# Performance work log

Hardware: AMD Instinct MI355X
Metric: run time of the kernel (lower is better)

Reference implementation:

```python
import jax, jax.numpy as jnp
import numpy as np

D = 1024
H = 16
FFN = 4096
B = 4
S = 1024
EPS = 1e-12
NEG = -1e9


def _layernorm(x, gamma, beta):
    mean = x.mean(-1, keepdims=True)
    var = ((x - mean) ** 2).mean(-1, keepdims=True)  # biased var, matches unbiased=False
    return gamma * (x - mean) * jax.lax.rsqrt(var + EPS) + beta


def setup_inputs() -> dict:
    key = jax.random.key(0)
    ks = jax.random.split(key, 16)
    s_in = 1.0 / np.sqrt(D)
    s_ff = 1.0 / np.sqrt(FFN)
    return {
        "x": jax.random.normal(ks[0], (B, S, D), dtype=jnp.float32),
        "mask": jax.random.randint(ks[1], (B, H, S), 0, 2) > 0,  # bernoulli(0.5) key mask
        "Wqkv": jax.random.uniform(ks[2], (3 * D, D), minval=-s_in, maxval=s_in),
        "bqkv": jax.random.uniform(ks[3], (3 * D,), minval=-s_in, maxval=s_in),
        "Wo": jax.random.uniform(ks[4], (D, D), minval=-s_in, maxval=s_in),
        "bo": jax.random.uniform(ks[5], (D,), minval=-s_in, maxval=s_in),
        "W1": jax.random.uniform(ks[6], (FFN, D), minval=-s_in, maxval=s_in),
        "b1": jax.random.uniform(ks[7], (FFN,), minval=-s_in, maxval=s_in),
        "W2": jax.random.uniform(ks[8], (D, FFN), minval=-s_ff, maxval=s_ff),
        "b2": jax.random.uniform(ks[9], (D,), minval=-s_ff, maxval=s_ff),
        "g1": jnp.ones((D,), jnp.float32),
        "be1": jnp.zeros((D,), jnp.float32),
        "g2": jnp.ones((D,), jnp.float32),
        "be2": jnp.zeros((D,), jnp.float32),
    }


def reference(x, mask, Wqkv, bqkv, Wo, bo, W1, b1, W2, b2, g1, be1, g2, be2):
    b, s, _ = x.shape
    hd = D // H
    scale = hd ** -0.5

    # --- ProbSparseSelfAttention (dropout in eval mode) ---
    qkv = x @ Wqkv.T + bqkv                                   # [b, s, 3D]
    q, k, v = jnp.split(qkv, 3, axis=-1)
    q = q.reshape(b, s, H, hd).transpose(0, 2, 1, 3)          # [b, h, s, d]
    k = k.reshape(b, s, H, hd).transpose(0, 2, 1, 3)
    v = v.reshape(b, s, H, hd).transpose(0, 2, 1, 3)
    scores = jnp.einsum('bhid,bhjd->bhij', q * scale, k)      # [b, h, s, s]
    scores = jnp.where(mask[:, :, None, :], scores, NEG)      # mask keys (broadcast over i)
    attn = jax.nn.softmax(scores, axis=-1)
    ctx = jnp.einsum('bhij,bhjd->bhid', attn, v)
    ctx = ctx.transpose(0, 2, 1, 3).reshape(b, s, D)
    attn_out = ctx @ Wo.T + bo

    # residual + LayerNorm 1
    h = _layernorm(attn_out + x, g1, be1)

    # --- FFN ---
    ff = jax.nn.relu(h @ W1.T + b1) @ W2.T + b2

    # residual + LayerNorm 2
    return _layernorm(ff + h, g2, be2)
```

## Files before the change

### kernel.cpp

```cpp
#include <hip/hip_runtime.h>

#define DDIM 1024
#define FFN_DIM 4096
#define SS 1024
#define MTOK 4096

typedef __bf16 bf16x8 __attribute__((ext_vector_type(8)));
typedef float f32x4 __attribute__((ext_vector_type(4)));
typedef unsigned short ushort4v __attribute__((ext_vector_type(4)));
typedef unsigned short ushort8v __attribute__((ext_vector_type(8)));

__device__ __forceinline__ unsigned short f2bf(float f) {
    __bf16 h = (__bf16)f;
    return __builtin_bit_cast(unsigned short, h);
}
__device__ __forceinline__ float bf2f(unsigned short u) {
    union { unsigned u; float f; } x;
    x.u = (unsigned)u << 16;
    return x.f;
}

__device__ __forceinline__ int swz(int off) {
    return off ^ ((((off >> 7) & 7) ^ ((off >> 10) & 1)) << 4);
}
__device__ __forceinline__ int gswz(int b) {
    return b ^ (((b >> 7) & 7) << 4);
}

__device__ __forceinline__ void gload_lds16(const void* g, void* l) {
    __builtin_amdgcn_global_load_lds(
        (__attribute__((address_space(1))) unsigned int*)(unsigned long long)(g),
        (__attribute__((address_space(3))) unsigned int*)(l), 16, 0, 0);
}

__global__ __launch_bounds__(256) void cvt_all(const float* __restrict__ x,
                                               const float* __restrict__ wqkv,
                                               const float* __restrict__ wo,
                                               const float* __restrict__ w1,
                                               const float* __restrict__ w2,
                                               unsigned short* __restrict__ xbf,
                                               unsigned short* __restrict__ wqkvb,
                                               unsigned short* __restrict__ wob,
                                               unsigned short* __restrict__ w1b,
                                               unsigned short* __restrict__ w2b) {
    int i = blockIdx.x * 256 + threadIdx.x;
    const float* src;
    unsigned short* dst;
    int off;
    if (i < 1048576)      { src = x;    dst = xbf;   off = i; }
    else if (i < 1835008) { src = wqkv; dst = wqkvb; off = i - 1048576; }
    else if (i < 2097152) { src = wo;   dst = wob;   off = i - 1835008; }
    else if (i < 3145728) { src = w1;   dst = w1b;   off = i - 2097152; }
    else                  { src = w2;   dst = w2b;   off = i - 3145728; }
    float4 v = ((const float4*)src)[off];
    ushort4v u = {f2bf(v.x), f2bf(v.y), f2bf(v.z), f2bf(v.w)};
    ((ushort4v*)dst)[off] = u;
}

template <int EPI, int SPLITK>
__global__ __launch_bounds__(512, 2) void gemm256(const unsigned short* __restrict__ A,
                                                  const unsigned short* __restrict__ B,
                                                  const float* __restrict__ bias,
                                                  unsigned short* __restrict__ O0,
                                                  unsigned short* __restrict__ O1,
                                                  unsigned short* __restrict__ O2,
                                                  unsigned short* __restrict__ O3,
                                                  int M, int N, int K) {
    __shared__ char smem[131072];
    const int tid = threadIdx.x;
    const int wid = tid >> 6, lane = tid & 63;
    const int wm = wid >> 2, wn = wid & 3;
    const int lr = lane & 15, lkb = (lane >> 4) * 16;
    const int m0 = blockIdx.y * 256, n0 = blockIdx.x * 256;
    const int z = blockIdx.z;
    const int Kc = K / SPLITK, kb = z * Kc;
    const int NT = Kc / 64;

    f32x4 acc[8][4];
#pragma unroll
    for (int i = 0; i < 8; i++)
#pragma unroll
        for (int j = 0; j < 4; j++) acc[i][j] = (f32x4){0.f, 0.f, 0.f, 0.f};

    auto stage_tile = [&](int c, int t) {
        const int k0 = kb + t * 64;
#pragma unroll
        for (int hs = 0; hs < 4; ++hs) {
            const int op = hs >> 1, h = hs & 1;
            const unsigned short* G = op ? B : A;
            const int r0 = (op ? n0 : m0) + h * 128;
            char* base = smem + c * 65536 + op * 32768 + h * 16384;
#pragma unroll
            for (int q = 0; q < 2; q++) {
                int d = q * 8192 + wid * 1024 + lane * 16;
                int s = gswz(d);
                gload_lds16(G + (size_t)(r0 + (s >> 7)) * K + k0 + ((s & 127) >> 1),
                            base + q * 8192 + wid * 1024);
            }
        }
    };

    stage_tile(0, 0);
    asm volatile("s_waitcnt vmcnt(0)" ::: "memory");
    __syncthreads();

    for (int t = 0; t < NT; ++t) {
        const int c = t & 1;
        const char* Ab = smem + c * 65536;
        const char* Bb = Ab + 32768;
        const bool pre = (t + 1 < NT);
        bf16x8 bfr[4][2];
#pragma unroll
        for (int p = 0; p < 4; ++p) {
            bf16x8 afr[2][2];
#pragma unroll
            for (int mi = 0; mi < 2; mi++)
#pragma unroll
                for (int ks = 0; ks < 2; ks++) {
                    int b = (wm * 128 + (p * 2 + mi) * 16 + lr) * 128 + ks * 64 + lkb;
                    afr[mi][ks] = *(const bf16x8*)(Ab + gswz(b));
                }
            if (p == 0) {
#pragma unroll
                for (int nb = 0; nb < 4; nb++)
#pragma unroll
                    for (int ks = 0; ks < 2; ks++) {
                        int b = (wn * 64 + nb * 16 + lr) * 128 + ks * 64 + lkb;
                        bfr[nb][ks] = *(const bf16x8*)(Bb + gswz(b));
                    }
                if (pre) stage_tile(c ^ 1, t + 1);
            }
            __builtin_amdgcn_s_barrier();
            asm volatile("s_waitcnt lgkmcnt(0)" ::: "memory");
            __builtin_amdgcn_sched_barrier(0);
            __builtin_amdgcn_s_setprio(1);
#pragma unroll
            for (int mi = 0; mi < 2; mi++)
#pragma unroll
                for (int nb = 0; nb < 4; nb++)
#pragma unroll
                    for (int ks = 0; ks < 2; ks++)
                        acc[p * 2 + mi][nb] = __builtin_amdgcn_mfma_f32_16x16x32_bf16(
                            afr[mi][ks], bfr[nb][ks], acc[p * 2 + mi][nb], 0, 0, 0);
            __builtin_amdgcn_s_setprio(0);
            if (p == 3 && pre) asm volatile("s_waitcnt vmcnt(0)" ::: "memory");
            __builtin_amdgcn_s_barrier();
        }
    }

    unsigned short* Op = (SPLITK == 1) ? O0 : (z == 0 ? O0 : z == 1 ? O1 : z == 2 ? O2 : O3);
    float bv[4];
#pragma unroll
    for (int nb = 0; nb < 4; nb++) bv[nb] = (z == 0) ? bias[n0 + wn * 64 + nb * 16 + lr] : 0.f;
    const int rr = (lane >> 4) * 4;
#pragma unroll
    for (int mb = 0; mb < 8; mb++)
#pragma unroll
        for (int nb = 0; nb < 4; nb++) {
            int col = n0 + wn * 64 + nb * 16 + lr;
#pragma unroll
            for (int r = 0; r < 4; r++) {
                int row = m0 + wm * 128 + mb * 16 + rr + r;
                float v = acc[mb][nb][r] + bv[nb];
                if (EPI == 2) v = fmaxf(v, 0.f);
                Op[(size_t)row * N + col] = f2bf(v);
            }
        }
}

__global__ __launch_bounds__(256) void gemm_bt(const unsigned short* __restrict__ A,
                                               const unsigned short* __restrict__ B,
                                               const float* __restrict__ bias,
                                               unsigned short* __restrict__ Cout,
                                               int M, int N, int K) {
    __shared__ unsigned short Asm[2][128 * 32];
    __shared__ unsigned short Bsm[2][128 * 32];
    const int tid = threadIdx.x;
    const int wid = tid >> 6, lane = tid & 63;
    const int m0 = blockIdx.y * 128, n0 = blockIdx.x * 128;
    const int lr = lane & 15, lk = (lane >> 4) * 8;
    const int wr = (wid >> 1) * 64, wc = (wid & 1) * 64;
    const int nkt = K / 32;

    f32x4 acc[4][4];
#pragma unroll
    for (int i = 0; i < 4; i++)
#pragma unroll
        for (int j = 0; j < 4; j++) acc[i][j] = (f32x4){0.f, 0.f, 0.f, 0.f};

    const unsigned short* Ag = A + (size_t)m0 * K;
    const unsigned short* Bg = B + (size_t)n0 * K;

    auto stage = [&](int buf, int k0) {
#pragma unroll
        for (int p = 0; p < 2; ++p) {
            int idx = p * 4096 + wid * 1024 + lane * 16;
            int row = idx >> 6, ce = (idx & 63) >> 1;
            gload_lds16(Ag + (size_t)row * K + k0 + ce, (char*)Asm[buf] + p * 4096 + wid * 1024);
            gload_lds16(Bg + (size_t)row * K + k0 + ce, (char*)Bsm[buf] + p * 4096 + wid * 1024);
        }
    };

    stage(0, 0);
    for (int kt = 0; kt < nkt; ++kt) {
        const int cur = kt & 1;
        __syncthreads();
        if (kt + 1 < nkt) stage(cur ^ 1, (kt + 1) * 32);
        bf16x8 af[4], bfr[4];
#pragma unroll
        for (int m = 0; m < 4; m++) af[m] = *(const bf16x8*)&Asm[cur][(wr + m * 16 + lr) * 32 + lk];
#pragma unroll
        for (int n = 0; n < 4; n++) bfr[n] = *(const bf16x8*)&Bsm[cur][(wc + n * 16 + lr) * 32 + lk];
#pragma unroll
        for (int m = 0; m < 4; m++)
#pragma unroll
            for (int n = 0; n < 4; n++)
                acc[m][n] = __builtin_amdgcn_mfma_f32_16x16x32_bf16(af[m], bfr[n], acc[m][n], 0, 0, 0);
    }

    float bv[4];
#pragma unroll
    for (int n = 0; n < 4; n++) bv[n] = bias[n0 + wc + n * 16 + lr];
    const int r0 = (lane >> 4) * 4;
#pragma unroll
    for (int m = 0; m < 4; m++)
#pragma unroll
        for (int n = 0; n < 4; n++) {
            int col = n0 + wc + n * 16 + lr;
#pragma unroll
            for (int r = 0; r < 4; r++) {
                int row = m0 + wr + m * 16 + r0 + r;
                Cout[(size_t)row * N + col] = f2bf(acc[m][n][r] + bv[n]);
            }
        }
}

__global__ __launch_bounds__(256) void vtrans(const unsigned short* __restrict__ qkv,
                                              unsigned short* __restrict__ vt) {
    __shared__ unsigned short T[64 * 64];
    const int tid = threadIdx.x;
    const int bh = blockIdx.y, b = bh >> 4, h = bh & 15;
    const int s0 = blockIdx.x * 64;
    const unsigned short* src = qkv + (size_t)(b * SS + s0) * 3072 + 2048 + h * 64;
#pragma unroll
    for (int p = 0; p < 2; p++) {
        int idx = p * 4096 + tid * 16;
        int row = idx >> 7, ce = (idx & 127) >> 1;
        ushort8v v = *(const ushort8v*)(src + (size_t)row * 3072 + ce);
        *(ushort8v*)((char*)T + swz(idx)) = v;
    }
    __syncthreads();
    unsigned short* dst = vt + (size_t)bh * 64 * SS + s0;
#pragma unroll
    for (int p = 0; p < 2; p++) {
        int idx = p * 4096 + tid * 16;
        int d = idx >> 7, t0 = (idx & 127) >> 1;
        ushort8v o;
#pragma unroll
        for (int i = 0; i < 8; i++)
            o[i] = *(const unsigned short*)((char*)T + swz((t0 + i) * 128 + d * 2));
        *(ushort8v*)(dst + (size_t)d * SS + t0) = o;
    }
}

__global__ __launch_bounds__(256) void attn_fused(const unsigned short* __restrict__ qkv,
                                                  const unsigned short* __restrict__ vt,
                                                  const int* __restrict__ mask,
                                                  unsigned short* __restrict__ ctx) {
    __shared__ unsigned short Ksm[2][64 * 64];
    __shared__ unsigned short Vsm[2][64 * 64];
    __shared__ unsigned short Psm[4][16 * 64];
    __shared__ float maskadd[2][64];
    const int tid = threadIdx.x, wid = tid >> 6, lane = tid & 63;
    const int bid = blockIdx.x;
    const int xcd = bid & 7, loc = bid >> 3;
    const int bh = xcd * 8 + (loc >> 4), q0 = (loc & 15) * 64;
    const int b = bh >> 4, h = bh & 15;
    const int lr = lane & 15, lk2 = (lane >> 4) * 16;
    const size_t base = (size_t)b * SS * 3072 + h * 64;
    const float SC2 = 0.18033688011112042f;

    bf16x8 qf[2];
    {
        const unsigned short* qp = qkv + base + (size_t)(q0 + wid * 16 + lr) * 3072;
        qf[0] = *(const bf16x8*)(qp + (lk2 >> 1));
        qf[1] = *(const bf16x8*)(qp + 32 + (lk2 >> 1));
    }
    float m_run[4] = {-3e38f, -3e38f, -3e38f, -3e38f};
    float l_run[4] = {0.f, 0.f, 0.f, 0.f};
    f32x4 oacc[4];
#pragma unroll
    for (int i = 0; i < 4; i++) oacc[i] = (f32x4){0.f, 0.f, 0.f, 0.f};

    const unsigned short* Kgb = qkv + base + 1024;
    const unsigned short* Vgb = vt + (size_t)bh * 64 * SS;

    auto stage = [&](int buf, int kt) {
#pragma unroll
        for (int p = 0; p < 2; p++) {
            int idx = p * 4096 + wid * 1024 + lane * 16;
            int s = swz(idx);
            int row = s >> 7, ce = (s & 127) >> 1;
            gload_lds16(Kgb + (size_t)(kt * 64 + row) * 3072 + ce,
                        (char*)Ksm[buf] + p * 4096 + wid * 1024);
            gload_lds16(Vgb + (size_t)row * SS + kt * 64 + ce,
                        (char*)Vsm[buf] + p * 4096 + wid * 1024);
        }
        if (tid < 64) maskadd[buf][tid] = mask[bh * SS + kt * 64 + tid] ? 0.f : -1.5e9f;
    };

    stage(0, 0);
    for (int kt = 0; kt < SS / 64; ++kt) {
        const int cur = kt & 1;
        __syncthreads();
        if (kt < SS / 64 - 1) stage(cur ^ 1, kt + 1);
        const char* Kb = (const char*)Ksm[cur];
        const char* Vb = (const char*)Vsm[cur];

        f32x4 sc[4];
#pragma unroll
        for (int nt = 0; nt < 4; nt++) {
            f32x4 a = (f32x4){0.f, 0.f, 0.f, 0.f};
            int rowb = (nt * 16 + lr) * 128;
            bf16x8 k0v = *(const bf16x8*)(Kb + swz(rowb + lk2));
            bf16x8 k1v = *(const bf16x8*)(Kb + swz(rowb + 64 + lk2));
            a = __builtin_amdgcn_mfma_f32_16x16x32_bf16(qf[0], k0v, a, 0, 0, 0);
            a = __builtin_amdgcn_mfma_f32_16x16x32_bf16(qf[1], k1v, a, 0, 0, 0);
            sc[nt] = a;
        }
        float mk[4];
#pragma unroll
        for (int nt = 0; nt < 4; nt++) mk[nt] = maskadd[cur][nt * 16 + lr];
        float pmax[4];
#pragma unroll
        for (int r = 0; r < 4; r++) {
            float v = -3e38f;
#pragma unroll
            for (int nt = 0; nt < 4; nt++) {
                float s = sc[nt][r] * SC2 + mk[nt];
                sc[nt][r] = s;
                v = fmaxf(v, s);
            }
            v = fmaxf(v, __shfl_xor(v, 1));
            v = fmaxf(v, __shfl_xor(v, 2));
            v = fmaxf(v, __shfl_xor(v, 4));
            v = fmaxf(v, __shfl_xor(v, 8));
            pmax[r] = v;
        }
        bool okt = true;
#pragma unroll
        for (int r = 0; r < 4; r++) okt = okt && (pmax[r] <= m_run[r] + 8.f);
        const bool skip = __all(okt);
        if (!skip) {
#pragma unroll
            for (int r = 0; r < 4; r++) {
                float mnew = fmaxf(m_run[r], pmax[r]);
                float alpha = exp2f(m_run[r] - mnew);
                m_run[r] = mnew;
                l_run[r] *= alpha;
#pragma unroll
                for (int dt = 0; dt < 4; dt++) oacc[dt][r] *= alpha;
            }
        }
#pragma unroll
        for (int r = 0; r < 4; r++) {
            float ls = 0.f;
#pragma unroll
            for (int nt = 0; nt < 4; nt++) {
                float pexp = exp2f(sc[nt][r] - m_run[r]);
                sc[nt][r] = pexp;
                ls += pexp;
            }
            ls += __shfl_xor(ls, 1);
            ls += __shfl_xor(ls, 2);
            ls += __shfl_xor(ls, 4);
            ls += __shfl_xor(ls, 8);
            l_run[r] += ls;
        }
        const int prow = (lane >> 4) * 4;
        char* Pb = (char*)Psm[wid];
#pragma unroll
        for (int nt = 0; nt < 4; nt++)
#pragma unroll
            for (int r = 0; r < 4; r++)
                *(unsigned short*)(Pb + swz((prow + r) * 128 + (nt * 16 + lr) * 2)) = f2bf(sc[nt][r]);
        bf16x8 pf0 = *(const bf16x8*)(Pb + swz(lr * 128 + lk2));
        bf16x8 pf1 = *(const bf16x8*)(Pb + swz(lr * 128 + 64 + lk2));
#pragma unroll
        for (int dt = 0; dt < 4; dt++) {
            int rowb = (dt * 16 + lr) * 128;
            bf16x8 v0 = *(const bf16x8*)(Vb + swz(rowb + lk2));
            bf16x8 v1 = *(const bf16x8*)(Vb + swz(rowb + 64 + lk2));
            oacc[dt] = __builtin_amdgcn_mfma_f32_16x16x32_bf16(pf0, v0, oacc[dt], 0, 0, 0);
            oacc[dt] = __builtin_amdgcn_mfma_f32_16x16x32_bf16(pf1, v1, oacc[dt], 0, 0, 0);
        }
    }
#pragma unroll
    for (int dt = 0; dt < 4; dt++)
#pragma unroll
        for (int r = 0; r < 4; r++) {
            float v = oacc[dt][r] / l_run[r];
            int row = q0 + wid * 16 + (lane >> 4) * 4 + r;
            ctx[(size_t)(b * SS + row) * DDIM + h * 64 + dt * 16 + lr] = f2bf(v);
        }
}

__global__ __launch_bounds__(256) void resid_ln1(const unsigned short* __restrict__ attno,
                                                 const float* __restrict__ x,
                                                 const float* __restrict__ gamma,
                                                 const float* __restrict__ beta,
                                                 unsigned short* __restrict__ hbf) {
    __shared__ float red[16];
    const int row = blockIdx.x, tid = threadIdx.x;
    const int wid = tid >> 6, lane = tid & 63;
    ushort4v av = ((const ushort4v*)(attno + (size_t)row * DDIM))[tid];
    float4 bv = ((const float4*)(x + (size_t)row * DDIM))[tid];
    float4 v;
    v.x = bf2f(av[0]) + bv.x; v.y = bf2f(av[1]) + bv.y;
    v.z = bf2f(av[2]) + bv.z; v.w = bf2f(av[3]) + bv.w;
    float s = v.x + v.y + v.z + v.w;
    float s2 = v.x * v.x + v.y * v.y + v.z * v.z + v.w * v.w;
#pragma unroll
    for (int off = 1; off < 64; off <<= 1) { s += __shfl_xor(s, off); s2 += __shfl_xor(s2, off); }
    if (lane == 0) { red[wid] = s; red[8 + wid] = s2; }
    __syncthreads();
    s = red[0] + red[1] + red[2] + red[3];
    s2 = red[8] + red[9] + red[10] + red[11];
    float mean = s * (1.f / 1024.f);
    float var = s2 * (1.f / 1024.f) - mean * mean;
    float rstd = rsqrtf(var + 1e-12f);
    float4 g = ((const float4*)gamma)[tid];
    float4 be = ((const float4*)beta)[tid];
    ushort4v u = {f2bf(g.x * (v.x - mean) * rstd + be.x),
                  f2bf(g.y * (v.y - mean) * rstd + be.y),
                  f2bf(g.z * (v.z - mean) * rstd + be.z),
                  f2bf(g.w * (v.w - mean) * rstd + be.w)};
    ((ushort4v*)(hbf + (size_t)row * DDIM))[tid] = u;
}

__global__ __launch_bounds__(256) void resid_ln2(const unsigned short* __restrict__ p0,
                                                 const unsigned short* __restrict__ p1,
                                                 const unsigned short* __restrict__ p2,
                                                 const unsigned short* __restrict__ p3,
                                                 const unsigned short* __restrict__ hbf,
                                                 const float* __restrict__ gamma,
                                                 const float* __restrict__ beta,
                                                 float* __restrict__ out) {
    __shared__ float red[16];
    const int row = blockIdx.x, tid = threadIdx.x;
    const int wid = tid >> 6, lane = tid & 63;
    size_t off = (size_t)row * DDIM;
    ushort4v a0 = ((const ushort4v*)(p0 + off))[tid];
    ushort4v a1 = ((const ushort4v*)(p1 + off))[tid];
    ushort4v a2 = ((const ushort4v*)(p2 + off))[tid];
    ushort4v a3 = ((const ushort4v*)(p3 + off))[tid];
    ushort4v hv = ((const ushort4v*)(hbf + off))[tid];
    float4 v;
    v.x = bf2f(a0[0]) + bf2f(a1[0]) + bf2f(a2[0]) + bf2f(a3[0]) + bf2f(hv[0]);
    v.y = bf2f(a0[1]) + bf2f(a1[1]) + bf2f(a2[1]) + bf2f(a3[1]) + bf2f(hv[1]);
    v.z = bf2f(a0[2]) + bf2f(a1[2]) + bf2f(a2[2]) + bf2f(a3[2]) + bf2f(hv[2]);
    v.w = bf2f(a0[3]) + bf2f(a1[3]) + bf2f(a2[3]) + bf2f(a3[3]) + bf2f(hv[3]);
    float s = v.x + v.y + v.z + v.w;
    float s2 = v.x * v.x + v.y * v.y + v.z * v.z + v.w * v.w;
#pragma unroll
    for (int off2 = 1; off2 < 64; off2 <<= 1) { s += __shfl_xor(s, off2); s2 += __shfl_xor(s2, off2); }
    if (lane == 0) { red[wid] = s; red[8 + wid] = s2; }
    __syncthreads();
    s = red[0] + red[1] + red[2] + red[3];
    s2 = red[8] + red[9] + red[10] + red[11];
    float mean = s * (1.f / 1024.f);
    float var = s2 * (1.f / 1024.f) - mean * mean;
    float rstd = rsqrtf(var + 1e-12f);
    float4 g = ((const float4*)gamma)[tid];
    float4 be = ((const float4*)beta)[tid];
    float4 o;
    o.x = g.x * (v.x - mean) * rstd + be.x;
    o.y = g.y * (v.y - mean) * rstd + be.y;
    o.z = g.z * (v.z - mean) * rstd + be.z;
    o.w = g.w * (v.w - mean) * rstd + be.w;
    ((float4*)(out + off))[tid] = o;
}

extern "C" void kernel_launch(void* const* d_in, const int* in_sizes, int n_in,
                              void* d_out, int out_size, void* d_ws, size_t ws_size,
                              hipStream_t stream) {
    const float* x    = (const float*)d_in[0];
    const int*   mask = (const int*)d_in[1];
    const float* Wqkv = (const float*)d_in[2];
    const float* bqkv = (const float*)d_in[3];
    const float* Wo   = (const float*)d_in[4];
    const float* bo   = (const float*)d_in[5];
    const float* W1   = (const float*)d_in[6];
    const float* b1   = (const float*)d_in[7];
    const float* W2   = (const float*)d_in[8];
    const float* b2   = (const float*)d_in[9];
    const float* g1   = (const float*)d_in[10];
    const float* be1  = (const float*)d_in[11];
    const float* g2   = (const float*)d_in[12];
    const float* be2  = (const float*)d_in[13];
    float* out = (float*)d_out;

    char* ws = (char*)d_ws;
    unsigned short* xbf   = (unsigned short*)(ws + 0);
    unsigned short* vtb   = (unsigned short*)(ws + 0);
    unsigned short* p0    = (unsigned short*)(ws + 0);
    unsigned short* qkvbf = (unsigned short*)(ws + (8ull << 20));
    unsigned short* ff1   = (unsigned short*)(ws + (8ull << 20));
    unsigned short* ctx   = (unsigned short*)(ws + (32ull << 20));
    unsigned short* w1b   = (unsigned short*)(ws + (40ull << 20));
    unsigned short* p1    = (unsigned short*)(ws + (40ull << 20));
    unsigned short* w2b   = (unsigned short*)(ws + (48ull << 20));
    unsigned short* wqkvb = (unsigned short*)(ws + (56ull << 20));
    unsigned short* p2    = (unsigned short*)(ws + (56ull << 20));
    unsigned short* wob   = (unsigned short*)(ws + (62ull << 20));
    unsigned short* attno = (unsigned short*)(ws + (64ull << 20));
    unsigned short* p3    = (unsigned short*)(ws + (64ull << 20));
    unsigned short* hbf   = (unsigned short*)(ws + (72ull << 20));

    cvt_all<<<16384, 256, 0, stream>>>(x, Wqkv, Wo, W1, W2, xbf, wqkvb, wob, w1b, w2b);

    gemm256<1, 1><<<dim3(12, 16, 1), 512, 0, stream>>>(xbf, wqkvb, bqkv,
        qkvbf, qkvbf, qkvbf, qkvbf, MTOK, 3072, 1024);
    vtrans<<<dim3(16, 64), 256, 0, stream>>>(qkvbf, vtb);
    attn_fused<<<1024, 256, 0, stream>>>(qkvbf, vtb, mask, ctx);
    gemm_bt<<<dim3(8, 32), 256, 0, stream>>>(ctx, wob, bo, attno, MTOK, 1024, 1024);
    resid_ln1<<<4096, 256, 0, stream>>>(attno, x, g1, be1, hbf);
    gemm256<2, 1><<<dim3(16, 16, 1), 512, 0, stream>>>(hbf, w1b, b1,
        ff1, ff1, ff1, ff1, MTOK, FFN_DIM, 1024);
    gemm256<1, 4><<<dim3(4, 16, 4), 512, 0, stream>>>(ff1, w2b, b2,
        p0, p1, p2, p3, MTOK, DDIM, FFN_DIM);
    resid_ln2<<<4096, 256, 0, stream>>>(p0, p1, p2, p3, hbf, g2, be2, out);
}
```

Baseline: 356.1 us.

## Replace GEMMs with triple-buffered 256x128 pipelined kernel and reduce split-K

Replaces the 256x256 double-buffered GEMM and the separate 128x128 GEMM with a single 256x128 tile kernel. It uses a three-stage LDS ring so two k-tiles are in flight and needs one barrier per k-step. The Wo projection now also uses this kernel with split-K of 2. The FFN2 split-K drops from 4 to 2, so the residual LayerNorm kernels read two partial buffers. Workspace offsets are rearranged to match. The aim is better latency hiding and fewer partial-sum bytes, at the cost of smaller tiles and more blocks.

```diff
diff --git a/kernel.cpp b/kernel.cpp
--- a/kernel.cpp
+++ b/kernel.cpp
@@ -58,179 +58,107 @@
 }
 
 template <int EPI, int SPLITK>
-__global__ __launch_bounds__(512, 2) void gemm256(const unsigned short* __restrict__ A,
-                                                  const unsigned short* __restrict__ B,
-                                                  const float* __restrict__ bias,
-                                                  unsigned short* __restrict__ O0,
-                                                  unsigned short* __restrict__ O1,
-                                                  unsigned short* __restrict__ O2,
-                                                  unsigned short* __restrict__ O3,
-                                                  int M, int N, int K) {
-    __shared__ char smem[131072];
+__global__ __launch_bounds__(512, 2) void gemm_pipe(const unsigned short* __restrict__ A,
+                                                    const unsigned short* __restrict__ B,
+                                                    const float* __restrict__ bias,
+                                                    unsigned short* __restrict__ O0,
+                                                    unsigned short* __restrict__ O1,
+                                                    int M, int N, int K) {
+    __shared__ char smem[3 * 49152];
     const int tid = threadIdx.x;
     const int wid = tid >> 6, lane = tid & 63;
-    const int wm = wid >> 2, wn = wid & 3;
+    const int wm = wid >> 1, wn = wid & 1;
     const int lr = lane & 15, lkb = (lane >> 4) * 16;
-    const int m0 = blockIdx.y * 256, n0 = blockIdx.x * 256;
+    const int m0 = blockIdx.y * 256, n0 = blockIdx.x * 128;
     const int z = blockIdx.z;
     const int Kc = K / SPLITK, kb = z * Kc;
     const int NT = Kc / 64;
 
-    f32x4 acc[8][4];
-#pragma unroll
-    for (int i = 0; i < 8; i++)
+    f32x4 acc[4][4];
+#pragma unroll
+    for (int i = 0; i < 4; i++)
 #pragma unroll
         for (int j = 0; j < 4; j++) acc[i][j] = (f32x4){0.f, 0.f, 0.f, 0.f};
 
-    auto stage_tile = [&](int c, int t) {
+    auto stage = [&](int buf, int t) {
         const int k0 = kb + t * 64;
-#pragma unroll
-        for (int hs = 0; hs < 4; ++hs) {
-            const int op = hs >> 1, h = hs & 1;
-            const unsigned short* G = op ? B : A;
-            const int r0 = (op ? n0 : m0) + h * 128;
-            char* base = smem + c * 65536 + op * 32768 + h * 16384;
-#pragma unroll
-            for (int q = 0; q < 2; q++) {
-                int d = q * 8192 + wid * 1024 + lane * 16;
-                int s = gswz(d);
-                gload_lds16(G + (size_t)(r0 + (s >> 7)) * K + k0 + ((s & 127) >> 1),
-                            base + q * 8192 + wid * 1024);
-            }
+        char* base = smem + buf * 49152;
+#pragma unroll
+        for (int q = 0; q < 4; q++) {
+            int d = q * 8192 + wid * 1024 + lane * 16;
+            int s = gswz(d);
+            gload_lds16(A + (size_t)(m0 + (s >> 7)) * K + k0 + ((s & 127) >> 1),
+                        base + q * 8192 + wid * 1024);
+        }
+#pragma unroll
+        for (int q = 0; q < 2; q++) {
+            int d = q * 8192 + wid * 1024 + lane * 16;
+            int s = gswz(d);
+            gload_lds16(B + (size_t)(n0 + (s >> 7)) * K + k0 + ((s & 127) >> 1),
+                        base + 32768 + q * 8192 + wid * 1024);
         }
     };
 
-    stage_tile(0, 0);
-    asm volatile("s_waitcnt vmcnt(0)" ::: "memory");
-    __syncthreads();
-
+    stage(0, 0);
+    if (NT > 1) stage(1, 1);
+
+    int cur = 0;
     for (int t = 0; t < NT; ++t) {
-        const int c = t & 1;
-        const char* Ab = smem + c * 65536;
+        if (t + 1 < NT) asm volatile("s_waitcnt vmcnt(6)" ::: "memory");
+        else            asm volatile("s_waitcnt vmcnt(0)" ::: "memory");
+        __builtin_amdgcn_s_barrier();
+        __builtin_amdgcn_sched_barrier(0);
+        if (t + 2 < NT) {
+            int nxt = cur + 2;
+            if (nxt >= 3) nxt -= 3;
+            stage(nxt, t + 2);
+        }
+        const char* Ab = smem + cur * 49152;
         const char* Bb = Ab + 32768;
-        const bool pre = (t + 1 < NT);
         bf16x8 bfr[4][2];
 #pragma unroll
-        for (int p = 0; p < 4; ++p) {
+        for (int nb = 0; nb < 4; nb++)
+#pragma unroll
+            for (int ks = 0; ks < 2; ks++)
+                bfr[nb][ks] = *(const bf16x8*)(Bb + gswz((wn * 64 + nb * 16 + lr) * 128 + ks * 64 + lkb));
+#pragma unroll
+        for (int half = 0; half < 2; half++) {
             bf16x8 afr[2][2];
 #pragma unroll
             for (int mi = 0; mi < 2; mi++)
 #pragma unroll
-                for (int ks = 0; ks < 2; ks++) {
-                    int b = (wm * 128 + (p * 2 + mi) * 16 + lr) * 128 + ks * 64 + lkb;
-                    afr[mi][ks] = *(const bf16x8*)(Ab + gswz(b));
-                }
-            if (p == 0) {
+                for (int ks = 0; ks < 2; ks++)
+                    afr[mi][ks] = *(const bf16x8*)(Ab + gswz((wm * 64 + (half * 2 + mi) * 16 + lr) * 128 + ks * 64 + lkb));
+            __builtin_amdgcn_s_setprio(1);
+#pragma unroll
+            for (int mi = 0; mi < 2; mi++)
 #pragma unroll
                 for (int nb = 0; nb < 4; nb++)
 #pragma unroll
-                    for (int ks = 0; ks < 2; ks++) {
-                        int b = (wn * 64 + nb * 16 + lr) * 128 + ks * 64 + lkb;
-                        bfr[nb][ks] = *(const bf16x8*)(Bb + gswz(b));
-                    }
-                if (pre) stage_tile(c ^ 1, t + 1);
-            }
-            __builtin_amdgcn_s_barrier();
-            asm volatile("s_waitcnt lgkmcnt(0)" ::: "memory");
-            __builtin_amdgcn_sched_barrier(0);
-            __builtin_amdgcn_s_setprio(1);
-#pragma unroll
-            for (int mi = 0; mi < 2; mi++)
-#pragma unroll
-                for (int nb = 0; nb < 4; nb++)
-#pragma unroll
                     for (int ks = 0; ks < 2; ks++)
-                        acc[p * 2 + mi][nb] = __builtin_amdgcn_mfma_f32_16x16x32_bf16(
-                            afr[mi][ks], bfr[nb][ks], acc[p * 2 + mi][nb], 0, 0, 0);
+                        acc[half * 2 + mi][nb] = __builtin_amdgcn_mfma_f32_16x16x32_bf16(
+                            afr[mi][ks], bfr[nb][ks], acc[half * 2 + mi][nb], 0, 0, 0);
             __builtin_amdgcn_s_setprio(0);
-            if (p == 3 && pre) asm volatile("s_waitcnt vmcnt(0)" ::: "memory");
-            __builtin_amdgcn_s_barrier();
-        }
+        }
+        cur = (cur == 2) ? 0 : cur + 1;
     }
 
-    unsigned short* Op = (SPLITK == 1) ? O0 : (z == 0 ? O0 : z == 1 ? O1 : z == 2 ? O2 : O3);
+    unsigned short* Op = (SPLITK == 1 || z == 0) ? O0 : O1;
     float bv[4];
 #pragma unroll
     for (int nb = 0; nb < 4; nb++) bv[nb] = (z == 0) ? bias[n0 + wn * 64 + nb * 16 + lr] : 0.f;
     const int rr = (lane >> 4) * 4;
 #pragma unroll
-    for (int mb = 0; mb < 8; mb++)
+    for (int mb = 0; mb < 4; mb++)
 #pragma unroll
         for (int nb = 0; nb < 4; nb++) {
             int col = n0 + wn * 64 + nb * 16 + lr;
 #pragma unroll
             for (int r = 0; r < 4; r++) {
-                int row = m0 + wm * 128 + mb * 16 + rr + r;
+                int row = m0 + wm * 64 + mb * 16 + rr + r;
                 float v = acc[mb][nb][r] + bv[nb];
                 if (EPI == 2) v = fmaxf(v, 0.f);
                 Op[(size_t)row * N + col] = f2bf(v);
-            }
-        }
-}
-
-__global__ __launch_bounds__(256) void gemm_bt(const unsigned short* __restrict__ A,
-                                               const unsigned short* __restrict__ B,
-                                               const float* __restrict__ bias,
-                                               unsigned short* __restrict__ Cout,
-                                               int M, int N, int K) {
-    __shared__ unsigned short Asm[2][128 * 32];
-    __shared__ unsigned short Bsm[2][128 * 32];
-    const int tid = threadIdx.x;
-    const int wid = tid >> 6, lane = tid & 63;
-    const int m0 = blockIdx.y * 128, n0 = blockIdx.x * 128;
-    const int lr = lane & 15, lk = (lane >> 4) * 8;
-    const int wr = (wid >> 1) * 64, wc = (wid & 1) * 64;
-    const int nkt = K / 32;
-
-    f32x4 acc[4][4];
-#pragma unroll
-    for (int i = 0; i < 4; i++)
-#pragma unroll
-        for (int j = 0; j < 4; j++) acc[i][j] = (f32x4){0.f, 0.f, 0.f, 0.f};
-
-    const unsigned short* Ag = A + (size_t)m0 * K;
-    const unsigned short* Bg = B + (size_t)n0 * K;
-
-    auto stage = [&](int buf, int k0) {
-#pragma unroll
-        for (int p = 0; p < 2; ++p) {
-            int idx = p * 4096 + wid * 1024 + lane * 16;
-            int row = idx >> 6, ce = (idx & 63) >> 1;
-            gload_lds16(Ag + (size_t)row * K + k0 + ce, (char*)Asm[buf] + p * 4096 + wid * 1024);
-            gload_lds16(Bg + (size_t)row * K + k0 + ce, (char*)Bsm[buf] + p * 4096 + wid * 1024);
-        }
-    };
-
-    stage(0, 0);
-    for (int kt = 0; kt < nkt; ++kt) {
-        const int cur = kt & 1;
-        __syncthreads();
-        if (kt + 1 < nkt) stage(cur ^ 1, (kt + 1) * 32);
-        bf16x8 af[4], bfr[4];
-#pragma unroll
-        for (int m = 0; m < 4; m++) af[m] = *(const bf16x8*)&Asm[cur][(wr + m * 16 + lr) * 32 + lk];
-#pragma unroll
-        for (int n = 0; n < 4; n++) bfr[n] = *(const bf16x8*)&Bsm[cur][(wc + n * 16 + lr) * 32 + lk];
-#pragma unroll
-        for (int m = 0; m < 4; m++)
-#pragma unroll
-            for (int n = 0; n < 4; n++)
-                acc[m][n] = __builtin_amdgcn_mfma_f32_16x16x32_bf16(af[m], bfr[n], acc[m][n], 0, 0, 0);
-    }
-
-    float bv[4];
-#pragma unroll
-    for (int n = 0; n < 4; n++) bv[n] = bias[n0 + wc + n * 16 + lr];
-    const int r0 = (lane >> 4) * 4;
-#pragma unroll
-    for (int m = 0; m < 4; m++)
-#pragma unroll
-        for (int n = 0; n < 4; n++) {
-            int col = n0 + wc + n * 16 + lr;
-#pragma unroll
-            for (int r = 0; r < 4; r++) {
-                int row = m0 + wr + m * 16 + r0 + r;
-                Cout[(size_t)row * N + col] = f2bf(acc[m][n][r] + bv[n]);
             }
         }
 }
@@ -405,7 +333,8 @@
         }
 }
 
-__global__ __launch_bounds__(256) void resid_ln1(const unsigned short* __restrict__ attno,
+__global__ __launch_bounds__(256) void resid_ln1(const unsigned short* __restrict__ wp0,
+                                                 const unsigned short* __restrict__ wp1,
                                                  const float* __restrict__ x,
                                                  const float* __restrict__ gamma,
                                                  const float* __restrict__ beta,
@@ -413,15 +342,19 @@
     __shared__ float red[16];
     const int row = blockIdx.x, tid = threadIdx.x;
     const int wid = tid >> 6, lane = tid & 63;
-    ushort4v av = ((const ushort4v*)(attno + (size_t)row * DDIM))[tid];
-    float4 bv = ((const float4*)(x + (size_t)row * DDIM))[tid];
+    size_t off = (size_t)row * DDIM;
+    ushort4v a0 = ((const ushort4v*)(wp0 + off))[tid];
+    ushort4v a1 = ((const ushort4v*)(wp1 + off))[tid];
+    float4 bv = ((const float4*)(x + off))[tid];
     float4 v;
-    v.x = bf2f(av[0]) + bv.x; v.y = bf2f(av[1]) + bv.y;
-    v.z = bf2f(av[2]) + bv.z; v.w = bf2f(av[3]) + bv.w;
+    v.x = bf2f(a0[0]) + bf2f(a1[0]) + bv.x;
+    v.y = bf2f(a0[1]) + bf2f(a1[1]) + bv.y;
+    v.z = bf2f(a0[2]) + bf2f(a1[2]) + bv.z;
+    v.w = bf2f(a0[3]) + bf2f(a1[3]) + bv.w;
     float s = v.x + v.y + v.z + v.w;
     float s2 = v.x * v.x + v.y * v.y + v.z * v.z + v.w * v.w;
 #pragma unroll
-    for (int off = 1; off < 64; off <<= 1) { s += __shfl_xor(s, off); s2 += __shfl_xor(s2, off); }
+    for (int o = 1; o < 64; o <<= 1) { s += __shfl_xor(s, o); s2 += __shfl_xor(s2, o); }
     if (lane == 0) { red[wid] = s; red[8 + wid] = s2; }
     __syncthreads();
     s = red[0] + red[1] + red[2] + red[3];
@@ -435,13 +368,11 @@
                   f2bf(g.y * (v.y - mean) * rstd + be.y),
                   f2bf(g.z * (v.z - mean) * rstd + be.z),
                   f2bf(g.w * (v.w - mean) * rstd + be.w)};
-    ((ushort4v*)(hbf + (size_t)row * DDIM))[tid] = u;
-}
-
-__global__ __launch_bounds__(256) void resid_ln2(const unsigned short* __restrict__ p0,
-                                                 const unsigned short* __restrict__ p1,
-                                                 const unsigned short* __restrict__ p2,
-                                                 const unsigned short* __restrict__ p3,
+    ((ushort4v*)(hbf + off))[tid] = u;
+}
+
+__global__ __launch_bounds__(256) void resid_ln2(const unsigned short* __restrict__ fp0,
+                                                 const unsigned short* __restrict__ fp1,
                                                  const unsigned short* __restrict__ hbf,
                                                  const float* __restrict__ gamma,
                                                  const float* __restrict__ beta,
@@ -450,20 +381,18 @@
     const int row = blockIdx.x, tid = threadIdx.x;
     const int wid = tid >> 6, lane = tid & 63;
     size_t off = (size_t)row * DDIM;
-    ushort4v a0 = ((const ushort4v*)(p0 + off))[tid];
-    ushort4v a1 = ((const ushort4v*)(p1 + off))[tid];
-    ushort4v a2 = ((const ushort4v*)(p2 + off))[tid];
-    ushort4v a3 = ((const ushort4v*)(p3 + off))[tid];
+    ushort4v a0 = ((const ushort4v*)(fp0 + off))[tid];
+    ushort4v a1 = ((const ushort4v*)(fp1 + off))[tid];
     ushort4v hv = ((const ushort4v*)(hbf + off))[tid];
     float4 v;
-    v.x = bf2f(a0[0]) + bf2f(a1[0]) + bf2f(a2[0]) + bf2f(a3[0]) + bf2f(hv[0]);
-    v.y = bf2f(a0[1]) + bf2f(a1[1]) + bf2f(a2[1]) + bf2f(a3[1]) + bf2f(hv[1]);
-    v.z = bf2f(a0[2]) + bf2f(a1[2]) + bf2f(a2[2]) + bf2f(a3[2]) + bf2f(hv[2]);
-    v.w = bf2f(a0[3]) + bf2f(a1[3]) + bf2f(a2[3]) + bf2f(a3[3]) + bf2f(hv[3]);
+    v.x = bf2f(a0[0]) + bf2f(a1[0]) + bf2f(hv[0]);
+    v.y = bf2f(a0[1]) + bf2f(a1[1]) + bf2f(hv[1]);
+    v.z = bf2f(a0[2]) + bf2f(a1[2]) + bf2f(hv[2]);
+    v.w = bf2f(a0[3]) + bf2f(a1[3]) + bf2f(hv[3]);
     float s = v.x + v.y + v.z + v.w;
     float s2 = v.x * v.x + v.y * v.y + v.z * v.z + v.w * v.w;
 #pragma unroll
-    for (int off2 = 1; off2 < 64; off2 <<= 1) { s += __shfl_xor(s, off2); s2 += __shfl_xor(s2, off2); }
+    for (int o = 1; o < 64; o <<= 1) { s += __shfl_xor(s, o); s2 += __shfl_xor(s2, o); }
     if (lane == 0) { red[wid] = s; red[8 + wid] = s2; }
     __syncthreads();
     s = red[0] + red[1] + red[2] + red[3];
@@ -503,31 +432,31 @@
     char* ws = (char*)d_ws;
     unsigned short* xbf   = (unsigned short*)(ws + 0);
     unsigned short* vtb   = (unsigned short*)(ws + 0);
-    unsigned short* p0    = (unsigned short*)(ws + 0);
+    unsigned short* ff1   = (unsigned short*)(ws + 0);
     unsigned short* qkvbf = (unsigned short*)(ws + (8ull << 20));
-    unsigned short* ff1   = (unsigned short*)(ws + (8ull << 20));
-    unsigned short* ctx   = (unsigned short*)(ws + (32ull << 20));
+    unsigned short* wp0   = (unsigned short*)(ws + (8ull << 20));
+    unsigned short* wp1   = (unsigned short*)(ws + (16ull << 20));
+    unsigned short* wqkvb = (unsigned short*)(ws + (32ull << 20));
+    unsigned short* hbf   = (unsigned short*)(ws + (32ull << 20));
+    unsigned short* wob   = (unsigned short*)(ws + (38ull << 20));
     unsigned short* w1b   = (unsigned short*)(ws + (40ull << 20));
-    unsigned short* p1    = (unsigned short*)(ws + (40ull << 20));
+    unsigned short* fp0   = (unsigned short*)(ws + (40ull << 20));
     unsigned short* w2b   = (unsigned short*)(ws + (48ull << 20));
-    unsigned short* wqkvb = (unsigned short*)(ws + (56ull << 20));
-    unsigned short* p2    = (unsigned short*)(ws + (56ull << 20));
-    unsigned short* wob   = (unsigned short*)(ws + (62ull << 20));
-    unsigned short* attno = (unsigned short*)(ws + (64ull << 20));
-    unsigned short* p3    = (unsigned short*)(ws + (64ull << 20));
-    unsigned short* hbf   = (unsigned short*)(ws + (72ull << 20));
+    unsigned short* ctx   = (unsigned short*)(ws + (56ull << 20));
+    unsigned short* fp1   = (unsigned short*)(ws + (56ull << 20));
 
     cvt_all<<<16384, 256, 0, stream>>>(x, Wqkv, Wo, W1, W2, xbf, wqkvb, wob, w1b, w2b);
 
-    gemm256<1, 1><<<dim3(12, 16, 1), 512, 0, stream>>>(xbf, wqkvb, bqkv,
-        qkvbf, qkvbf, qkvbf, qkvbf, MTOK, 3072, 1024);
+    gemm_pipe<1, 1><<<dim3(24, 16, 1), 512, 0, stream>>>(xbf, wqkvb, bqkv, qkvbf, qkvbf,
+                                                         MTOK, 3072, 1024);
     vtrans<<<dim3(16, 64), 256, 0, stream>>>(qkvbf, vtb);
     attn_fused<<<1024, 256, 0, stream>>>(qkvbf, vtb, mask, ctx);
-    gemm_bt<<<dim3(8, 32), 256, 0, stream>>>(ctx, wob, bo, attno, MTOK, 1024, 1024);
-    resid_ln1<<<4096, 256, 0, stream>>>(attno, x, g1, be1, hbf);
-    gemm256<2, 1><<<dim3(16, 16, 1), 512, 0, stream>>>(hbf, w1b, b1,
-        ff1, ff1, ff1, ff1, MTOK, FFN_DIM, 1024);
-    gemm256<1, 4><<<dim3(4, 16, 4), 512, 0, stream>>>(ff1, w2b, b2,
-        p0, p1, p2, p3, MTOK, DDIM, FFN_DIM);
-    resid_ln2<<<4096, 256, 0, stream>>>(p0, p1, p2, p3, hbf, g2, be2, out);
-}
+    gemm_pipe<1, 2><<<dim3(8, 16, 2), 512, 0, stream>>>(ctx, wob, bo, wp0, wp1,
+                                                        MTOK, 1024, 1024);
+    resid_ln1<<<4096, 256, 0, stream>>>(wp0, wp1, x, g1, be1, hbf);
+    gemm_pipe<2, 1><<<dim3(32, 16, 1), 512, 0, stream>>>(hbf, w1b, b1, ff1, ff1,
+                                                         MTOK, FFN_DIM, 1024);
+    gemm_pipe<1, 2><<<dim3(8, 16, 2), 512, 0, stream>>>(ff1, w2b, b2, fp0, fp1,
+                                                        MTOK, DDIM, FFN_DIM);
+    resid_ln2<<<4096, 256, 0, stream>>>(fp0, fp1, hbf, g2, be2, out);
+}
```

Measured after the change: 358.5 us. Within noise of the previous version (+0.7%).
